# Optimization experiments

Measured on AMD Instinct MI355X. Metric: run time of the kernel, lower is better.

## Reference

```python
import jax, jax.numpy as jnp
import numpy as np

SCORE_THR = 0.5
IOU_THR = 0.5
N_ANCHORS = 8400  # standard YOLO 640x640 anchor count


def setup_inputs() -> dict:
    key = jax.random.key(0)
    # [1, 5, N]: channels are (cx, cy, w, h, person_conf); uniform keeps boxes/scores in [0,1)
    yolo_raw_out = jax.random.uniform(key, (1, 5, N_ANCHORS), dtype=jnp.float32)
    return {"yolo_raw_out": yolo_raw_out}


def _pairwise_iou(b):
    # b: [N,4] xyxy
    area = (b[:, 2] - b[:, 0]) * (b[:, 3] - b[:, 1])          # [N]
    lt = jnp.maximum(b[:, None, :2], b[None, :, :2])          # [N,N,2]
    rb = jnp.minimum(b[:, None, 2:], b[None, :, 2:])          # [N,N,2]
    wh = jnp.clip(rb - lt, 0.0)
    inter = wh[..., 0] * wh[..., 1]                           # [N,N]
    union = area[:, None] + area[None, :] - inter
    return inter / jnp.maximum(union, 1e-9)


def reference(yolo_raw_out):
    # permute(0,2,1).squeeze(0) -> [N,5]
    raw = yolo_raw_out[0].T
    cx, cy, w, h = raw[:, 0], raw[:, 1], raw[:, 2], raw[:, 3]
    scores = raw[:, 4]
    # cxcywh -> xyxy (torchvision.ops.box_convert)
    xyxy = jnp.stack([cx - w / 2, cy - h / 2, cx + w / 2, cy + h / 2], axis=-1)

    valid = scores >= SCORE_THR
    # sort by score descending; invalid boxes pushed to the end
    order = jnp.argsort(-jnp.where(valid, scores, -jnp.inf))
    sb = xyxy[order]          # [N,4] sorted boxes
    ss = scores[order]        # [N]
    sv = valid[order]         # [N] score-threshold mask

    iou = _pairwise_iou(sb)   # [N,N]
    n = ss.shape[0]
    idx = jnp.arange(n)

    # Greedy NMS: in score order, an active (kept, valid) box suppresses all
    # lower-scored boxes with IoU > threshold. Faithful to torchvision.ops.nms.
    def step(keep, i):
        active = keep[i]
        suppress = (iou[i] > IOU_THR) & (idx > i) & active
        return keep & ~suppress, None

    keep, _ = jax.lax.scan(step, sv, idx)

    # Fixed-shape output: kept rows carry (x1,y1,x2,y2,score); suppressed/filtered rows zeroed.
    out = jnp.concatenate([sb, ss[:, None]], axis=1) * keep[:, None].astype(ss.dtype)
    return out
```

## Files before the change

kernel.cpp:

```cpp
#include <hip/hip_runtime.h>
#include <cstdint>

#define N_ANCH 8400
#define CBLK 132
#define SCORE_THR 0.5f

typedef unsigned long long u64;
typedef unsigned int u32;

__device__ __forceinline__ u64 sort_key(float s, int idx) {
  u32 k32 = (s >= SCORE_THR) ? ~__float_as_uint(s) : 0xFFFFFFFFu;
  return ((u64)k32 << 32) | (u32)idx;
}

__device__ __forceinline__ u64 readlane_u64(u64 v, int l) {
  u32 rlo = (u32)__builtin_amdgcn_readlane((int)(u32)v, l);
  u32 rhi = (u32)__builtin_amdgcn_readlane((int)(u32)(v >> 32), l);
  return ((u64)rhi << 32) | rlo;
}

__device__ __forceinline__ u64 rfl64(u64 v) {
  u32 lo = (u32)__builtin_amdgcn_readfirstlane((int)(u32)v);
  u32 hi = (u32)__builtin_amdgcn_readfirstlane((int)(u32)(v >> 32));
  return ((u64)hi << 32) | lo;
}

__global__ void __launch_bounds__(256) rank_kernel(const float* __restrict__ raw,
                                                   float4* __restrict__ sbox,
                                                   float* __restrict__ sscore) {
  #pragma clang fp contract(off)
  int tid = blockIdx.x * 256 + threadIdx.x;
  int row = tid >> 6, lane = tid & 63;
  if (row >= N_ANCH) return;
  float si = raw[4 * N_ANCH + row];
  u64 ki = sort_key(si, row);
  int cnt = 0;
  for (int j = lane; j < N_ANCH; j += 64) {
    float sj = raw[4 * N_ANCH + j];
    cnt += (sort_key(sj, j) < ki) ? 1 : 0;
  }
  #pragma unroll
  for (int d = 1; d < 64; d <<= 1) cnt += __shfl_xor(cnt, d, 64);
  if (lane == 0) {
    float cx = raw[row], cy = raw[N_ANCH + row];
    float w = raw[2 * N_ANCH + row], h = raw[3 * N_ANCH + row];
    float hw = w * 0.5f, hh = h * 0.5f;
    sbox[cnt] = make_float4(cx - hw, cy - hh, cx + hw, cy + hh);
    sscore[cnt] = si;
  }
}

__global__ void __launch_bounds__(256) mask_kernel(const float4* __restrict__ sbox,
                                                   const float* __restrict__ sscore,
                                                   u64* __restrict__ mask) {
  #pragma clang fp contract(off)
  int cb = blockIdx.x;
  int i0 = blockIdx.y * 256;
  if (cb * 64 + 63 < i0) return;
  if (!(sscore[i0] >= SCORE_THR)) return;
  if (!(sscore[cb * 64] >= SCORE_THR)) return;
  int t = threadIdx.x;
  __shared__ float4 cbox[64];
  __shared__ float carea[64];
  int j0 = cb * 64;
  if (t < 64) {
    int j = j0 + t;
    float4 bj = (j < N_ANCH) ? sbox[j] : make_float4(0.f, 0.f, 0.f, 0.f);
    cbox[t] = bj;
    carea[t] = (bj.z - bj.x) * (bj.w - bj.y);
  }
  __syncthreads();
  int i = i0 + t;
  if (i >= N_ANCH || i >= (cb + 1) * 64) return;
  float4 bi = sbox[i];
  float ai = (bi.z - bi.x) * (bi.w - bi.y);
  u64 word = 0;
  for (int jj = 0; jj < 64; ++jj) {
    int jg = j0 + jj;
    if (jg <= i || jg >= N_ANCH) continue;
    float4 bb = cbox[jj];
    float ltx = fmaxf(bi.x, bb.x), lty = fmaxf(bi.y, bb.y);
    float rbx = fminf(bi.z, bb.z), rby = fminf(bi.w, bb.w);
    float wx = fmaxf(rbx - ltx, 0.f), wy = fmaxf(rby - lty, 0.f);
    float inter = wx * wy;
    float uni = (ai + carea[jj]) - inter;
    float iou = inter / fmaxf(uni, 1e-9f);
    if (iou > 0.5f) word |= (1ull << jj);
  }
  mask[(u64)i * CBLK + cb] = word;
}

__global__ void __launch_bounds__(512, 1) nms_kernel(const float4* __restrict__ sbox,
                                                     const float* __restrict__ sscore,
                                                     const u64* __restrict__ mask,
                                                     float* __restrict__ out) {
  __shared__ u64 keepw[CBLK];
  __shared__ u64 rem7[7][CBLK];
  int tid = threadIdx.x;
  int wave = tid >> 6, lane = tid & 63;

  float s0 = sscore[lane * 132];
  u64 pb = __ballot(s0 >= SCORE_THR);
  int cnt1 = (int)__popcll(pb);
  int n_valid = 0;
  if (cnt1 > 0) {
    int a = (cnt1 - 1) * 132 + 1;
    int i1 = a + 3 * lane;
    float t1 = (i1 + 0 < N_ANCH) ? sscore[i1 + 0] : -1.f;
    float t2 = (i1 + 1 < N_ANCH) ? sscore[i1 + 1] : -1.f;
    float t3 = (i1 + 2 < N_ANCH) ? sscore[i1 + 2] : -1.f;
    u64 q1 = __ballot(t1 >= SCORE_THR);
    u64 q2 = __ballot(t2 >= SCORE_THR);
    u64 q3 = __ballot(t3 >= SCORE_THR);
    n_valid = a + (int)__popcll(q1) + (int)__popcll(q2) + (int)__popcll(q3);
  }
  int VB = (n_valid + 63) >> 6;
  int NT = (VB + 1) >> 1;

  for (int b = tid; b < CBLK; b += 512) keepw[b] = 0;
  for (int x = tid; x < 7 * CBLK; x += 512) ((u64*)rem7)[x] = 0;

  int rs = (wave - 1) * 19;
  int nr = 128 - rs; if (nr > 19) nr = 19;
  u64 tl[19], th[19];
  auto issue_tiles = [&](int u) {
    int cL = 2 * u + 4 + lane;
    int cH = cL + 64;
    bool okL = (cL < VB), okH = (cH < VB);
    const u64* pr = mask + (u64)(128 * u + rs) * CBLK;
    #pragma unroll
    for (int r = 0; r < 19; ++r) {
      bool rok = (r < nr);
      tl[r] = (rok && okL) ? pr[(u64)r * CBLK + cL] : 0ull;
      th[r] = (rok && okH) ? pr[(u64)r * CBLK + cH] : 0ull;
    }
  };

  u64 A_c=0,B_c=0,C_c=0,D0_c=0,D1_c=0,E0_c=0,E1_c=0;
  u64 A_n=0,B_n=0,C_n=0,D0_n=0,D1_n=0,E0_n=0,E1_n=0;
  auto load_w0 = [&](int T, u64&A,u64&B,u64&C,u64&D0,u64&D1,u64&E0,u64&E1) {
    int b0 = 2 * T, b1 = 2 * T + 1;
    int r0 = b0 * 64 + lane;
    int r1 = b1 * 64 + lane;
    if (r1 > N_ANCH - 1) r1 = N_ANCH - 1;
    bool ok1 = (b1 < VB);
    bool ok2 = (b0 + 2 < VB);
    bool ok3 = (b0 + 3 < VB);
    const u64* p0 = mask + (u64)r0 * CBLK;
    const u64* p1 = mask + (u64)r1 * CBLK;
    A  = p0[b0];
    B  = ok1 ? p0[b1] : 0ull;
    C  = ok1 ? p1[b1] : 0ull;
    D0 = ok2 ? p0[b0 + 2] : 0ull;
    D1 = ok3 ? p0[b0 + 3] : 0ull;
    E0 = (ok1 && ok2) ? p1[b0 + 2] : 0ull;
    E1 = (ok1 && ok3) ? p1[b0 + 3] : 0ull;
  };

  u64 carry0 = 0, carry1 = 0;

  if (wave == 0 && NT > 0) load_w0(0, A_c,B_c,C_c,D0_c,D1_c,E0_c,E1_c);

  for (int T = 0; T < NT; ++T) {
    asm volatile("s_waitcnt lgkmcnt(0)\ns_barrier" ::: "memory");

    if (wave == 0) {
      if (T > 0) { A_c=A_n; B_c=B_n; C_c=C_n; D0_c=D0_n; D1_c=D1_n; E0_c=E0_n; E1_c=E1_n; }
      if (T + 1 < NT) load_w0(T + 1, A_n,B_n,C_n,D0_n,D1_n,E0_n,E1_n);

      int b0 = 2 * T, b1 = 2 * T + 1;
      u64 r0v = carry0, r1v = carry1;
      #pragma unroll
      for (int j = 0; j < 7; ++j) { r0v |= rem7[j][b0]; r1v |= rem7[j][b1]; }
      u64 remb0 = rfl64(r0v);
      u64 remb1 = rfl64(r1v);
      int remn0 = n_valid - b0 * 64;
      int remn1 = remn0 - 64;
      u64 vm0 = (remn0 >= 64) ? ~0ull : ((1ull << remn0) - 1ull);
      u64 vm1 = (remn1 >= 64) ? ~0ull
              : ((remn1 <= 0) ? 0ull : ((1ull << remn1) - 1ull));
      u64 act0 = vm0 & ~remb0;
      u64 act1 = vm1 & ~remb1;

      u64 sup0 = __ballot((((act0 >> lane) & 1ull) != 0ull) &&
                          ((A_c | B_c) != 0ull));
      u64 a0v = act0, a1v = act1, k0 = 0, as;
      while ((as = a0v & sup0) != 0ull) {
        int f = (int)__builtin_ctzll(as);
        u64 bit = as & (0ull - as);
        u64 ml0 = readlane_u64(A_c, f);
        u64 ml1 = readlane_u64(B_c, f);
        k0 |= bit;
        a0v &= ~(bit | ml0);
        a1v &= ~ml1;
      }
      u64 kw0 = a0v | k0;

      u64 sup1 = __ballot((((act1 >> lane) & 1ull) != 0ull) && (C_c != 0ull));
      u64 k1 = 0;
      while ((as = a1v & sup1) != 0ull) {
        int f = (int)__builtin_ctzll(as);
        u64 bit = as & (0ull - as);
        u64 ml = readlane_u64(C_c, f);
        k1 |= bit;
        a1v &= ~(bit | ml);
      }
      u64 kw1 = a1v | k1;

      if (lane == 0) { keepw[b0] = kw0; keepw[b1] = kw1; }

      u64 kb0 = (kw0 >> lane) & 1ull;
      u64 kb1 = (kw1 >> lane) & 1ull;
      u64 x0 = (kb0 ? D0_c : 0ull) | (kb1 ? E0_c : 0ull);
      u64 x1 = (kb0 ? D1_c : 0ull) | (kb1 ? E1_c : 0ull);
      #pragma unroll
      for (int d = 1; d < 64; d <<= 1) {
        x0 |= __shfl_xor(x0, d, 64);
        x1 |= __shfl_xor(x1, d, 64);
      }
      carry0 = x0; carry1 = x1;
    } else {
      if (T > 0) {
        int u = T - 1;
        u64 kws0 = rfl64(keepw[2 * u]);
        u64 kws1 = rfl64(keepw[2 * u + 1]);
        u64 accL = 0, accH = 0;
        #pragma unroll
        for (int r = 0; r < 19; ++r) {
          int rr = rs + r;
          u64 bit = (rr < 64) ? (kws0 >> rr) : (kws1 >> (rr - 64));
          u64 sm = (u64)0 - (bit & 1ull);
          accL |= tl[r] & sm;
          accH |= th[r] & sm;
        }
        int cL = 2 * u + 4 + lane, cH = cL + 64;
        if (cL < VB) rem7[wave - 1][cL] |= accL;
        if (cH < VB) rem7[wave - 1][cH] |= accH;
      }
      if (T + 1 < NT) issue_tiles(T);
    }
  }
  __syncthreads();

  for (int r2 = tid; r2 < N_ANCH; r2 += 512) {
    u64 kv = keepw[r2 >> 6];
    bool kp = (kv >> (r2 & 63)) & 1ull;
    float4 b4 = sbox[r2];
    float sc = sscore[r2];
    float* o = out + r2 * 5;
    o[0] = kp ? b4.x : 0.f;
    o[1] = kp ? b4.y : 0.f;
    o[2] = kp ? b4.z : 0.f;
    o[3] = kp ? b4.w : 0.f;
    o[4] = kp ? sc : 0.f;
  }
}

extern "C" void kernel_launch(void* const* d_in, const int* in_sizes, int n_in,
                              void* d_out, int out_size, void* d_ws, size_t ws_size,
                              hipStream_t stream) {
  const float* raw = (const float*)d_in[0];
  float* out = (float*)d_out;
  char* ws = (char*)d_ws;
  float4* sbox = (float4*)ws;
  float* sscore = (float*)(ws + 8448 * 16);
  u64* mask = (u64*)(ws + 8448 * 16 + 8448 * 4);

  rank_kernel<<<2100, 256, 0, stream>>>(raw, sbox, sscore);
  mask_kernel<<<dim3(CBLK, 33), 256, 0, stream>>>(sbox, sscore, mask);
  nms_kernel<<<1, 512, 0, stream>>>(sbox, sscore, mask, out);
}
```

Measured before the change: 159.4 us.

## Resolve intra-block NMS with ballot rounds using transposed lower-triangular mask

The mask kernel now fills every block, storing lower-triangular (who-suppresses-me) words for diagonal and below-diagonal blocks. Wave 0 uses these to settle each 64-box block with a few ballot rounds instead of a serial readlane loop per kept box. Cross-block carries become single ballots instead of shuffle-OR reductions. The seven per-wave removal arrays merge into one shared array updated with LDS atomicOr. The cost is roughly double the IoU work and mask writes in mask_kernel.

```diff
diff --git a/kernel.cpp b/kernel.cpp
--- a/kernel.cpp
+++ b/kernel.cpp
@@ -11,12 +11,6 @@
 __device__ __forceinline__ u64 sort_key(float s, int idx) {
   u32 k32 = (s >= SCORE_THR) ? ~__float_as_uint(s) : 0xFFFFFFFFu;
   return ((u64)k32 << 32) | (u32)idx;
-}
-
-__device__ __forceinline__ u64 readlane_u64(u64 v, int l) {
-  u32 rlo = (u32)__builtin_amdgcn_readlane((int)(u32)v, l);
-  u32 rhi = (u32)__builtin_amdgcn_readlane((int)(u32)(v >> 32), l);
-  return ((u64)rhi << 32) | rlo;
 }
 
 __device__ __forceinline__ u64 rfl64(u64 v) {
@@ -56,7 +50,6 @@
   #pragma clang fp contract(off)
   int cb = blockIdx.x;
   int i0 = blockIdx.y * 256;
-  if (cb * 64 + 63 < i0) return;
   if (!(sscore[i0] >= SCORE_THR)) return;
   if (!(sscore[cb * 64] >= SCORE_THR)) return;
   int t = threadIdx.x;
@@ -71,13 +64,12 @@
   }
   __syncthreads();
   int i = i0 + t;
-  if (i >= N_ANCH || i >= (cb + 1) * 64) return;
+  if (i >= N_ANCH) return;
   float4 bi = sbox[i];
   float ai = (bi.z - bi.x) * (bi.w - bi.y);
-  u64 word = 0;
+  u64 wHi = 0, wLo = 0;
   for (int jj = 0; jj < 64; ++jj) {
     int jg = j0 + jj;
-    if (jg <= i || jg >= N_ANCH) continue;
     float4 bb = cbox[jj];
     float ltx = fmaxf(bi.x, bb.x), lty = fmaxf(bi.y, bb.y);
     float rbx = fminf(bi.z, bb.z), rby = fminf(bi.w, bb.w);
@@ -85,17 +77,19 @@
     float inter = wx * wy;
     float uni = (ai + carea[jj]) - inter;
     float iou = inter / fmaxf(uni, 1e-9f);
-    if (iou > 0.5f) word |= (1ull << jj);
-  }
-  mask[(u64)i * CBLK + cb] = word;
+    bool sup = (iou > 0.5f) && (jg < N_ANCH);
+    wHi |= (u64)(sup && (jg > i)) << jj;
+    wLo |= (u64)(sup && (jg < i)) << jj;
+  }
+  mask[(u64)i * CBLK + cb] = (cb > (i >> 6)) ? wHi : wLo;
 }
 
 __global__ void __launch_bounds__(512, 1) nms_kernel(const float4* __restrict__ sbox,
                                                      const float* __restrict__ sscore,
                                                      const u64* __restrict__ mask,
                                                      float* __restrict__ out) {
-  __shared__ u64 keepw[CBLK];
-  __shared__ u64 rem7[7][CBLK];
+  __shared__ u64 keepw[CBLK + 2];
+  __shared__ u64 rem[CBLK + 2];
   int tid = threadIdx.x;
   int wave = tid >> 6, lane = tid & 63;
 
@@ -117,8 +111,7 @@
   int VB = (n_valid + 63) >> 6;
   int NT = (VB + 1) >> 1;
 
-  for (int b = tid; b < CBLK; b += 512) keepw[b] = 0;
-  for (int x = tid; x < 7 * CBLK; x += 512) ((u64*)rem7)[x] = 0;
+  for (int b = tid; b < CBLK + 2; b += 512) { keepw[b] = 0; rem[b] = 0; }
 
   int rs = (wave - 1) * 19;
   int nr = 128 - rs; if (nr > 19) nr = 19;
@@ -136,44 +129,43 @@
     }
   };
 
-  u64 A_c=0,B_c=0,C_c=0,D0_c=0,D1_c=0,E0_c=0,E1_c=0;
-  u64 A_n=0,B_n=0,C_n=0,D0_n=0,D1_n=0,E0_n=0,E1_n=0;
-  auto load_w0 = [&](int T, u64&A,u64&B,u64&C,u64&D0,u64&D1,u64&E0,u64&E1) {
-    int b0 = 2 * T, b1 = 2 * T + 1;
+  u64 cA=0,cB=0,cC=0,cD0=0,cD1=0,cE0=0,cE1=0;
+  u64 nA=0,nB=0,nC=0,nD0=0,nD1=0,nE0=0,nE1=0;
+  auto load_w0 = [&](int T2, u64&A,u64&B,u64&C,u64&D0,u64&D1,u64&E0,u64&E1) {
+    int b0 = 2 * T2, b1 = b0 + 1;
     int r0 = b0 * 64 + lane;
-    int r1 = b1 * 64 + lane;
-    if (r1 > N_ANCH - 1) r1 = N_ANCH - 1;
-    bool ok1 = (b1 < VB);
-    bool ok2 = (b0 + 2 < VB);
-    bool ok3 = (b0 + 3 < VB);
+    int r1 = b1 * 64 + lane; if (r1 > N_ANCH - 1) r1 = N_ANCH - 1;
+    int r2 = (b0 + 2) * 64 + lane; if (r2 > N_ANCH - 1) r2 = N_ANCH - 1;
+    int r3 = (b0 + 3) * 64 + lane; if (r3 > N_ANCH - 1) r3 = N_ANCH - 1;
+    bool ok1 = (b1 < VB), ok2 = (b0 + 2 < VB), ok3 = (b0 + 3 < VB);
     const u64* p0 = mask + (u64)r0 * CBLK;
     const u64* p1 = mask + (u64)r1 * CBLK;
+    const u64* p2 = mask + (u64)r2 * CBLK;
+    const u64* p3 = mask + (u64)r3 * CBLK;
     A  = p0[b0];
-    B  = ok1 ? p0[b1] : 0ull;
+    B  = ok1 ? p1[b0] : 0ull;
     C  = ok1 ? p1[b1] : 0ull;
-    D0 = ok2 ? p0[b0 + 2] : 0ull;
-    D1 = ok3 ? p0[b0 + 3] : 0ull;
-    E0 = (ok1 && ok2) ? p1[b0 + 2] : 0ull;
-    E1 = (ok1 && ok3) ? p1[b0 + 3] : 0ull;
+    D0 = ok2 ? p2[b0] : 0ull;
+    D1 = ok2 ? p2[b1] : 0ull;
+    E0 = ok3 ? p3[b0] : 0ull;
+    E1 = ok3 ? p3[b1] : 0ull;
   };
 
   u64 carry0 = 0, carry1 = 0;
 
-  if (wave == 0 && NT > 0) load_w0(0, A_c,B_c,C_c,D0_c,D1_c,E0_c,E1_c);
+  if (wave == 0 && NT > 0) load_w0(0, cA,cB,cC,cD0,cD1,cE0,cE1);
 
   for (int T = 0; T < NT; ++T) {
     asm volatile("s_waitcnt lgkmcnt(0)\ns_barrier" ::: "memory");
 
     if (wave == 0) {
-      if (T > 0) { A_c=A_n; B_c=B_n; C_c=C_n; D0_c=D0_n; D1_c=D1_n; E0_c=E0_n; E1_c=E1_n; }
-      if (T + 1 < NT) load_w0(T + 1, A_n,B_n,C_n,D0_n,D1_n,E0_n,E1_n);
-
-      int b0 = 2 * T, b1 = 2 * T + 1;
-      u64 r0v = carry0, r1v = carry1;
-      #pragma unroll
-      for (int j = 0; j < 7; ++j) { r0v |= rem7[j][b0]; r1v |= rem7[j][b1]; }
-      u64 remb0 = rfl64(r0v);
-      u64 remb1 = rfl64(r1v);
+      int b0 = 2 * T, b1 = b0 + 1;
+      u64 rb0 = rem[b0], rb1 = rem[b1];
+      if (T > 0) { cA=nA; cB=nB; cC=nC; cD0=nD0; cD1=nD1; cE0=nE0; cE1=nE1; }
+      if (T + 1 < NT) load_w0(T + 1, nA,nB,nC,nD0,nD1,nE0,nE1);
+
+      u64 remb0 = rfl64(rb0 | carry0);
+      u64 remb1 = rfl64(rb1 | carry1);
       int remn0 = n_valid - b0 * 64;
       int remn1 = remn0 - 64;
       u64 vm0 = (remn0 >= 64) ? ~0ull : ((1ull << remn0) - 1ull);
@@ -182,43 +174,31 @@
       u64 act0 = vm0 & ~remb0;
       u64 act1 = vm1 & ~remb1;
 
-      u64 sup0 = __ballot((((act0 >> lane) & 1ull) != 0ull) &&
-                          ((A_c | B_c) != 0ull));
-      u64 a0v = act0, a1v = act1, k0 = 0, as;
-      while ((as = a0v & sup0) != 0ull) {
-        int f = (int)__builtin_ctzll(as);
-        u64 bit = as & (0ull - as);
-        u64 ml0 = readlane_u64(A_c, f);
-        u64 ml1 = readlane_u64(B_c, f);
-        k0 |= bit;
-        a0v &= ~(bit | ml0);
-        a1v &= ~ml1;
+      u64 U = act0, K0 = 0;
+      while (U) {
+        u64 covered = __ballot((cA & U) != 0ull);
+        u64 nk = U & ~covered;
+        u64 supp = __ballot((cA & nk) != 0ull);
+        K0 |= nk;
+        U &= ~(nk | supp);
       }
-      u64 kw0 = a0v | k0;
-
-      u64 sup1 = __ballot((((act1 >> lane) & 1ull) != 0ull) && (C_c != 0ull));
-      u64 k1 = 0;
-      while ((as = a1v & sup1) != 0ull) {
-        int f = (int)__builtin_ctzll(as);
-        u64 bit = as & (0ull - as);
-        u64 ml = readlane_u64(C_c, f);
-        k1 |= bit;
-        a1v &= ~(bit | ml);
+      u64 kw0 = K0;
+
+      u64 s01 = __ballot((cB & kw0) != 0ull);
+      u64 U1 = act1 & ~s01, K1 = 0;
+      while (U1) {
+        u64 covered = __ballot((cC & U1) != 0ull);
+        u64 nk = U1 & ~covered;
+        u64 supp = __ballot((cC & nk) != 0ull);
+        K1 |= nk;
+        U1 &= ~(nk | supp);
       }
-      u64 kw1 = a1v | k1;
+      u64 kw1 = K1;
 
       if (lane == 0) { keepw[b0] = kw0; keepw[b1] = kw1; }
 
-      u64 kb0 = (kw0 >> lane) & 1ull;
-      u64 kb1 = (kw1 >> lane) & 1ull;
-      u64 x0 = (kb0 ? D0_c : 0ull) | (kb1 ? E0_c : 0ull);
-      u64 x1 = (kb0 ? D1_c : 0ull) | (kb1 ? E1_c : 0ull);
-      #pragma unroll
-      for (int d = 1; d < 64; d <<= 1) {
-        x0 |= __shfl_xor(x0, d, 64);
-        x1 |= __shfl_xor(x1, d, 64);
-      }
-      carry0 = x0; carry1 = x1;
+      carry0 = __ballot(((cD0 & kw0) | (cD1 & kw1)) != 0ull);
+      carry1 = __ballot(((cE0 & kw0) | (cE1 & kw1)) != 0ull);
     } else {
       if (T > 0) {
         int u = T - 1;
@@ -234,8 +214,8 @@
           accH |= th[r] & sm;
         }
         int cL = 2 * u + 4 + lane, cH = cL + 64;
-        if (cL < VB) rem7[wave - 1][cL] |= accL;
-        if (cH < VB) rem7[wave - 1][cH] |= accH;
+        if (cL < VB && accL) atomicOr((unsigned long long*)&rem[cL], accL);
+        if (cH < VB && accH) atomicOr((unsigned long long*)&rem[cH], accH);
       }
       if (T + 1 < NT) issue_tiles(T);
     }
```

Measured after the change: 174.1 us. 1.09x slower.
